# Kernel optimization log

Measured on AMD Instinct MI355X. Metric: run time of the kernel, lower is better.

Reference implementation:

```python
import jax, jax.numpy as jnp
import numpy as np

B, S, D, H = 4, 2048, 1024, 16
HD = D // H  # head dim = 64


def setup_inputs() -> dict:
    key = jax.random.key(0)
    k1, k2, k3 = jax.random.split(key, 3)
    scale = 1.0 / np.sqrt(D).astype(np.float32)
    x = jax.random.normal(k1, (B, S, D), dtype=jnp.float32)
    # q/k slices of nn.MultiheadAttention's in_proj (v and out_proj never
    # influence the returned values since x_t is discarded by forward)
    wq = jax.random.normal(k2, (D, D), dtype=jnp.float32) * scale
    wk = jax.random.normal(k3, (D, D), dtype=jnp.float32) * scale
    bq = jnp.zeros((D,), dtype=jnp.float32)
    bk = jnp.zeros((D,), dtype=jnp.float32)
    # 8 contiguous scale blocks of 256 tokens; last boundary == S
    scales_idx = (jnp.arange(1, 9, dtype=jnp.int64) * (S // 8))
    return {"x": x, "wq": wq, "wk": wk, "bq": bq, "bk": bk,
            "scales_idx": scales_idx}


def reference(x, wq, wk, bq, bk, scales_idx):
    b, s, d = x.shape
    # project q, k and split heads: [B, H, S, HD]
    q = (x @ wq.T + bq).reshape(b, s, H, HD).transpose(0, 2, 1, 3)
    k = (x @ wk.T + bk).reshape(b, s, H, HD).transpose(0, 2, 1, 3)
    inv_sqrt_hd = jnp.asarray(1.0 / np.sqrt(HD), dtype=x.dtype)
    scores = jnp.einsum('bhqd,bhkd->bhqk', q, k) * inv_sqrt_hd  # [B,H,S,S]
    # block-diagonal mask: token i belongs to the block whose right boundary
    # is the first scales_idx entry strictly greater than i
    pos = jnp.arange(s)
    seg = jnp.searchsorted(scales_idx, pos, side='right')  # [S]
    allowed = seg[:, None] == seg[None, :]                  # [S,S] bool
    scores = jnp.where(allowed[None, None], scores, -jnp.inf)
    w = jax.nn.softmax(scores, axis=-1)  # every row has >=1 allowed entry
    weights_attn = jnp.mean(w, axis=1)   # average over heads -> [B,S,S]
    return (x, weights_attn)
```

## Files before the change

kernel.cpp:

```cpp
#include <hip/hip_runtime.h>
#include <hip/hip_bf16.h>
#include <math.h>

#define BB 4
#define SS 2048
#define DD 1024
#define HH 16
#define HD 64
#define MM (BB*SS)
#define NN (2*DD)
#define BK 64
#define NKT 16

typedef __attribute__((ext_vector_type(8))) short short8;
typedef __attribute__((ext_vector_type(4))) float f32x4;
typedef unsigned short ushort_t;

__device__ __forceinline__ void gload16(const void* g, void* l) {
    __builtin_amdgcn_global_load_lds((const __attribute__((address_space(1))) unsigned int*)g,
                                     (__attribute__((address_space(3))) unsigned int*)l,
                                     16, 0, 0);
}

__global__ __launch_bounds__(256)
void copy_cast(const float* __restrict__ x, float* __restrict__ out_x,
               __hip_bfloat16* __restrict__ xb, int n8)
{
    int i = blockIdx.x * 256 + threadIdx.x;
    if (i >= n8) return;
    const float4* s = (const float4*)x + (size_t)i * 2;
    float4 a = s[0], b = s[1];
    float4* o = (float4*)out_x + (size_t)i * 2;
    o[0] = a; o[1] = b;
    __hip_bfloat16 tmp[8];
    tmp[0] = __float2bfloat16(a.x); tmp[1] = __float2bfloat16(a.y);
    tmp[2] = __float2bfloat16(a.z); tmp[3] = __float2bfloat16(a.w);
    tmp[4] = __float2bfloat16(b.x); tmp[5] = __float2bfloat16(b.y);
    tmp[6] = __float2bfloat16(b.z); tmp[7] = __float2bfloat16(b.w);
    *(float4*)&xb[(size_t)i * 8] = *(float4*)tmp;
}

__global__ __launch_bounds__(256)
void cast_w(const float* __restrict__ wq, const float* __restrict__ wk,
            __hip_bfloat16* __restrict__ wb)
{
    const int half = (DD * DD) / 8;
    int i = blockIdx.x * 256 + threadIdx.x;
    if (i >= 2 * half) return;
    const float* src = (i < half) ? wq : wk;
    int j = (i < half) ? i : i - half;
    const float4* s = (const float4*)src + (size_t)j * 2;
    float4 a = s[0], b = s[1];
    __hip_bfloat16 tmp[8];
    tmp[0] = __float2bfloat16(a.x); tmp[1] = __float2bfloat16(a.y);
    tmp[2] = __float2bfloat16(a.z); tmp[3] = __float2bfloat16(a.w);
    tmp[4] = __float2bfloat16(b.x); tmp[5] = __float2bfloat16(b.y);
    tmp[6] = __float2bfloat16(b.z); tmp[7] = __float2bfloat16(b.w);
    *(float4*)&wb[(size_t)i * 8] = *(float4*)tmp;
}

__device__ __forceinline__ void stage_A(const ushort_t* __restrict__ xb, ushort_t* Ab,
                                        int m0, int kt, int mh, int wv, int lane)
{
    #pragma unroll
    for (int it = 0; it < 2; ++it) {
        int rl0 = it * 64 + wv * 8;
        int r0 = (rl0 & 63) + ((rl0 >> 6) << 7) + mh * 64;
        int r  = r0 + (lane >> 3);
        int gch = (lane & 7) ^ (r & 7);
        gload16(xb + (size_t)(m0 + r) * DD + kt + gch * 8, Ab + r0 * 64);
    }
}

__device__ __forceinline__ void stage_Bt(const ushort_t* __restrict__ wb, ushort_t* Bb,
                                         int n0, int kt, int nh, int wv, int lane)
{
    #pragma unroll
    for (int it = 0; it < 2; ++it) {
        int rl0 = it * 64 + wv * 8;
        int r0 = (rl0 & 31) + ((rl0 >> 5) << 6) + nh * 32;
        int r  = r0 + (lane >> 3);
        int gch = (lane & 7) ^ (r & 7);
        gload16(wb + (size_t)(n0 + r) * DD + kt + gch * 8, Bb + r0 * 64);
    }
}

__global__ __launch_bounds__(512, 2)
void proj_mfma(const ushort_t* __restrict__ xb, const ushort_t* __restrict__ wb,
               const float* __restrict__ bq, const float* __restrict__ bk,
               __hip_bfloat16* __restrict__ Qb, __hip_bfloat16* __restrict__ Kb)
{
    __shared__ __align__(16) ushort_t As[2][256 * BK];
    __shared__ __align__(16) ushort_t Bs[2][256 * BK];

    const int t = threadIdx.x;
    const int wv = t >> 6, lane = t & 63, quad = lane >> 4, l15 = lane & 15;
    const int wr = wv >> 2, wc = wv & 3;
    const int m0 = blockIdx.x * 256, n0 = blockIdx.y * 256;

    f32x4 acc[8][4];
    #pragma unroll
    for (int mt = 0; mt < 8; ++mt)
        #pragma unroll
        for (int nt = 0; nt < 4; ++nt) acc[mt][nt] = (f32x4){0.f, 0.f, 0.f, 0.f};

    stage_Bt(wb, Bs[0], n0, 0, 0, wv, lane);
    stage_A (xb, As[0], m0, 0, 0, wv, lane);
    stage_A (xb, As[0], m0, 0, 1, wv, lane);
    stage_Bt(wb, Bs[0], n0, 0, 1, wv, lane);
    stage_Bt(wb, Bs[1], n0, BK, 0, wv, lane);
    stage_A (xb, As[1], m0, BK, 0, wv, lane);
    asm volatile("s_waitcnt vmcnt(4)" ::: "memory");
    __builtin_amdgcn_s_barrier();

    #pragma unroll 1
    for (int tt = 0; tt < NKT; ++tt) {
        ushort_t* Ac = As[tt & 1];
        ushort_t* Bc = Bs[tt & 1];
        ushort_t* An = As[(tt & 1) ^ 1];
        ushort_t* Bn = Bs[(tt & 1) ^ 1];
        short8 a[8][2], b[2][2];

        #pragma unroll
        for (int mt = 0; mt < 4; ++mt)
            #pragma unroll
            for (int ks = 0; ks < 2; ++ks) {
                int r = wr * 128 + mt * 16 + l15;
                int sl = r * 8 + ((ks * 4 + quad) ^ (r & 7));
                a[mt][ks] = *(const short8*)&Ac[sl * 8];
            }
        #pragma unroll
        for (int nt = 0; nt < 2; ++nt)
            #pragma unroll
            for (int ks = 0; ks < 2; ++ks) {
                int r = wc * 64 + nt * 16 + l15;
                int sl = r * 8 + ((ks * 4 + quad) ^ (r & 7));
                b[nt][ks] = *(const short8*)&Bc[sl * 8];
            }
        if (tt + 1 < NKT) stage_A(xb, An, m0, (tt + 1) * BK, 1, wv, lane);
        __builtin_amdgcn_s_barrier();
        asm volatile("s_waitcnt lgkmcnt(0)" ::: "memory");
        __builtin_amdgcn_sched_barrier(0);
        __builtin_amdgcn_s_setprio(1);
        #pragma unroll
        for (int mt = 0; mt < 4; ++mt)
            #pragma unroll
            for (int nt = 0; nt < 2; ++nt)
                #pragma unroll
                for (int ks = 0; ks < 2; ++ks)
                    acc[mt][nt] = __builtin_amdgcn_mfma_f32_16x16x32_bf16(
                        a[mt][ks], b[nt][ks], acc[mt][nt], 0, 0, 0);
        __builtin_amdgcn_s_setprio(0);
        __builtin_amdgcn_sched_barrier(0);
        __builtin_amdgcn_s_barrier();

        #pragma unroll
        for (int mt = 0; mt < 4; ++mt)
            #pragma unroll
            for (int ks = 0; ks < 2; ++ks) {
                int r = wr * 128 + 64 + mt * 16 + l15;
                int sl = r * 8 + ((ks * 4 + quad) ^ (r & 7));
                a[4 + mt][ks] = *(const short8*)&Ac[sl * 8];
            }
        if (tt + 1 < NKT) stage_Bt(wb, Bn, n0, (tt + 1) * BK, 1, wv, lane);
        __builtin_amdgcn_s_barrier();
        asm volatile("s_waitcnt lgkmcnt(0)" ::: "memory");
        __builtin_amdgcn_sched_barrier(0);
        __builtin_amdgcn_s_setprio(1);
        #pragma unroll
        for (int mt = 0; mt < 4; ++mt)
            #pragma unroll
            for (int nt = 0; nt < 2; ++nt)
                #pragma unroll
                for (int ks = 0; ks < 2; ++ks)
                    acc[4 + mt][nt] = __builtin_amdgcn_mfma_f32_16x16x32_bf16(
                        a[4 + mt][ks], b[nt][ks], acc[4 + mt][nt], 0, 0, 0);
        __builtin_amdgcn_s_setprio(0);
        __builtin_amdgcn_sched_barrier(0);
        __builtin_amdgcn_s_barrier();

        #pragma unroll
        for (int nt = 0; nt < 2; ++nt)
            #pragma unroll
            for (int ks = 0; ks < 2; ++ks) {
                int r = wc * 64 + 32 + nt * 16 + l15;
                int sl = r * 8 + ((ks * 4 + quad) ^ (r & 7));
                b[nt][ks] = *(const short8*)&Bc[sl * 8];
            }
        if (tt + 2 < NKT) stage_Bt(wb, Bc, n0, (tt + 2) * BK, 0, wv, lane);
        __builtin_amdgcn_s_barrier();
        asm volatile("s_waitcnt lgkmcnt(0)" ::: "memory");
        __builtin_amdgcn_sched_barrier(0);
        __builtin_amdgcn_s_setprio(1);
        #pragma unroll
        for (int mt = 0; mt < 4; ++mt)
            #pragma unroll
            for (int nt = 0; nt < 2; ++nt)
                #pragma unroll
                for (int ks = 0; ks < 2; ++ks)
                    acc[mt][2 + nt] = __builtin_amdgcn_mfma_f32_16x16x32_bf16(
                        a[mt][ks], b[nt][ks], acc[mt][2 + nt], 0, 0, 0);
        __builtin_amdgcn_s_setprio(0);
        __builtin_amdgcn_sched_barrier(0);
        __builtin_amdgcn_s_barrier();

        if (tt + 2 < NKT) stage_A(xb, Ac, m0, (tt + 2) * BK, 0, wv, lane);
        __builtin_amdgcn_s_barrier();
        asm volatile("s_waitcnt lgkmcnt(0)" ::: "memory");
        __builtin_amdgcn_sched_barrier(0);
        __builtin_amdgcn_s_setprio(1);
        #pragma unroll
        for (int mt = 0; mt < 4; ++mt)
            #pragma unroll
            for (int nt = 0; nt < 2; ++nt)
                #pragma unroll
                for (int ks = 0; ks < 2; ++ks)
                    acc[4 + mt][2 + nt] = __builtin_amdgcn_mfma_f32_16x16x32_bf16(
                        a[4 + mt][ks], b[nt][ks], acc[4 + mt][2 + nt], 0, 0, 0);
        __builtin_amdgcn_s_setprio(0);
        __builtin_amdgcn_sched_barrier(0);
        if (tt < NKT - 2)       asm volatile("s_waitcnt vmcnt(4)" ::: "memory");
        else if (tt == NKT - 2) asm volatile("s_waitcnt vmcnt(0)" ::: "memory");
        __builtin_amdgcn_s_barrier();
    }

    const bool isQ = (n0 < DD);
    const float* bias = isQ ? bq : bk;
    __hip_bfloat16* outp = isQ ? Qb : Kb;
    const int nc0 = (isQ ? n0 : n0 - DD) + wc * 64;
    #pragma unroll
    for (int nt = 0; nt < 4; ++nt) {
        const int nc = nc0 + nt * 16 + l15;
        const float bv = bias[nc];
        #pragma unroll
        for (int mt = 0; mt < 8; ++mt)
            #pragma unroll
            for (int reg = 0; reg < 4; ++reg) {
                int m = m0 + wr * 128 + mt * 16 + quad * 4 + reg;
                outp[(size_t)m * DD + nc] = __float2bfloat16(acc[mt][nt][reg] + bv);
            }
    }
}

__global__ __launch_bounds__(256, 1)
void attn_block(const ushort_t* __restrict__ Qb, const ushort_t* __restrict__ Kb,
                const int* __restrict__ scales, float* __restrict__ outw)
{
    __shared__ __align__(16) char smem[73728];
    ushort_t* KsB = (ushort_t*)smem;
    ushort_t* QsB = (ushort_t*)(smem + 65536);
    float (*comb)[256] = (float(*)[256])smem;

    const int bid = blockIdx.x;
    const int rt  = bid >> 5;
    const int blk = bid & 7, bb = (bid >> 3) & 3;
    const int start = blk ? scales[blk - 1] : 0;

    const int t = threadIdx.x;
    const int wv = t >> 6, lane = t & 63, quad = lane >> 4, l15 = lane & 15;
    const int rg = wv & 1, hg = wv >> 1;

    f32x4 accm[16];
    #pragma unroll
    for (int nt = 0; nt < 16; ++nt) accm[nt] = (f32x4){0.f, 0.f, 0.f, 0.f};

    const int qrow0 = start + rt * 32;

    for (int i = 0; i < 8; ++i) {
        __syncthreads();
        #pragma unroll
        for (int half = 0; half < 2; ++half) {
            const int h = half * 8 + i;
            ushort_t* Kl = KsB + half * (256 * 64);
            ushort_t* Ql = QsB + half * (32 * 64);
            #pragma unroll
            for (int round = 0; round < 8; ++round) {
                int c = round * 256 + t;
                int row = c >> 3, ch = c & 7;
                int gch = ch ^ (row & 7);
                gload16(Kb + (size_t)(bb * SS + start + row) * DD + h * HD + gch * 8,
                        Kl + ((size_t)round * 256 + wv * 64) * 8);
            }
            {
                int row = t >> 3, ch = t & 7;
                int gch = ch ^ (row & 7);
                gload16(Qb + (size_t)(bb * SS + qrow0 + row) * DD + h * HD + gch * 8,
                        Ql + ((size_t)wv * 64) * 8);
            }
        }
        __syncthreads();

        const ushort_t* Ks = KsB + hg * (256 * 64);
        const ushort_t* Qs = QsB + hg * (32 * 64);

        short8 af[2];
        #pragma unroll
        for (int ks = 0; ks < 2; ++ks) {
            int qr = rg * 16 + l15;
            int sl = qr * 8 + ((ks * 4 + quad) ^ (qr & 7));
            af[ks] = *(const short8*)&Qs[sl * 8];
        }
        f32x4 sc[16];
        #pragma unroll
        for (int nt = 0; nt < 16; ++nt) {
            sc[nt] = (f32x4){0.f, 0.f, 0.f, 0.f};
            #pragma unroll
            for (int ks = 0; ks < 2; ++ks) {
                int kr = nt * 16 + l15;
                int sl = kr * 8 + ((ks * 4 + quad) ^ (kr & 7));
                short8 bf = *(const short8*)&Ks[sl * 8];
                sc[nt] = __builtin_amdgcn_mfma_f32_16x16x32_bf16(af[ks], bf, sc[nt], 0, 0, 0);
            }
        }
        float rs[4] = {0.f, 0.f, 0.f, 0.f};
        #pragma unroll
        for (int nt = 0; nt < 16; ++nt) {
            #pragma unroll
            for (int r = 0; r < 4; ++r) {
                float p = __expf(sc[nt][r] * 0.125f);
                sc[nt][r] = p;
                rs[r] += p;
            }
        }
        #pragma unroll
        for (int r = 0; r < 4; ++r) {
            #pragma unroll
            for (int off = 1; off < 16; off <<= 1) rs[r] += __shfl_xor(rs[r], off, 64);
            rs[r] = 1.0f / rs[r];
        }
        #pragma unroll
        for (int nt = 0; nt < 16; ++nt)
            #pragma unroll
            for (int r = 0; r < 4; ++r) accm[nt][r] += sc[nt][r] * rs[r];
    }

    __syncthreads();
    if (hg == 0) {
        #pragma unroll
        for (int nt = 0; nt < 16; ++nt)
            #pragma unroll
            for (int r = 0; r < 4; ++r)
                comb[rg * 16 + quad * 4 + r][nt * 16 + l15] = accm[nt][r];
    }
    __syncthreads();
    if (hg == 1) {
        #pragma unroll
        for (int nt = 0; nt < 16; ++nt)
            #pragma unroll
            for (int r = 0; r < 4; ++r)
                comb[rg * 16 + quad * 4 + r][nt * 16 + l15] += accm[nt][r];
    }
    __syncthreads();

    const float s16 = 1.0f / (float)HH;
    const size_t orow0 = (size_t)bb * SS + qrow0;
    #pragma unroll
    for (int it = 0; it < 64; ++it) {
        int flat = it * 256 + t;
        int row = flat >> 9;
        int col = (flat & 511) * 4;
        float4 v = make_float4(0.f, 0.f, 0.f, 0.f);
        unsigned lc = (unsigned)(col - start);
        if (lc < 256u) {
            const float* c = &comb[row][lc];
            v = make_float4(c[0] * s16, c[1] * s16, c[2] * s16, c[3] * s16);
        }
        *(float4*)&outw[(orow0 + row) * SS + col] = v;
    }
}

extern "C" void kernel_launch(void* const* d_in, const int* in_sizes, int n_in,
                              void* d_out, int out_size, void* d_ws, size_t ws_size,
                              hipStream_t stream)
{
    const float* x  = (const float*)d_in[0];
    const float* wq = (const float*)d_in[1];
    const float* wk = (const float*)d_in[2];
    const float* bq = (const float*)d_in[3];
    const float* bk = (const float*)d_in[4];
    const int* scales = (const int*)d_in[5];

    float* out_x = (float*)d_out;
    float* out_w = out_x + (size_t)BB * SS * DD;

    char* w = (char*)d_ws;
    __hip_bfloat16* xb = (__hip_bfloat16*)(w);
    __hip_bfloat16* wb = (__hip_bfloat16*)(w + 16777216);
    __hip_bfloat16* Qb = (__hip_bfloat16*)(w + 20971520);
    __hip_bfloat16* Kb = (__hip_bfloat16*)(w + 37748736);

    copy_cast<<<4096, 256, 0, stream>>>(x, out_x, xb, (MM * DD) / 8);
    cast_w<<<1024, 256, 0, stream>>>(wq, wk, wb);

    dim3 pgrid(MM / 256, NN / 256);
    proj_mfma<<<pgrid, 512, 0, stream>>>((const ushort_t*)xb, (const ushort_t*)wb,
                                         bq, bk, Qb, Kb);

    attn_block<<<256, 256, 0, stream>>>((const ushort_t*)Qb, (const ushort_t*)Kb,
                                        scales, out_w);
}
```

Before: 208.0 us.

## Double-buffer K/Q staging in attention kernel and use nontemporal output stores

The attention kernel now double-buffers the per-head K and Q tiles in LDS, issuing the next head's async global-to-LDS loads before computing the current head, with a partial vmcnt wait and raw barriers in place of __syncthreads. This aims to hide global load latency behind MFMA and softmax work. Separately, the x copy and the large weights output use nontemporal stores to reduce cache pollution on streaming writes. LDS use doubles to 144 KB, which removes any chance of a second block per CU, and the hand-tuned vmcnt count depends on the exact number of loads issued per stage.

```diff
diff --git a/kernel.cpp b/kernel.cpp
--- a/kernel.cpp
+++ b/kernel.cpp
@@ -28,10 +28,11 @@
 {
     int i = blockIdx.x * 256 + threadIdx.x;
     if (i >= n8) return;
-    const float4* s = (const float4*)x + (size_t)i * 2;
-    float4 a = s[0], b = s[1];
-    float4* o = (float4*)out_x + (size_t)i * 2;
-    o[0] = a; o[1] = b;
+    const f32x4* s = (const f32x4*)x + (size_t)i * 2;
+    f32x4 a = s[0], b = s[1];
+    f32x4* o = (f32x4*)out_x + (size_t)i * 2;
+    __builtin_nontemporal_store(a, o);
+    __builtin_nontemporal_store(b, o + 1);
     __hip_bfloat16 tmp[8];
     tmp[0] = __float2bfloat16(a.x); tmp[1] = __float2bfloat16(a.y);
     tmp[2] = __float2bfloat16(a.z); tmp[3] = __float2bfloat16(a.w);
@@ -246,9 +247,7 @@
 void attn_block(const ushort_t* __restrict__ Qb, const ushort_t* __restrict__ Kb,
                 const int* __restrict__ scales, float* __restrict__ outw)
 {
-    __shared__ __align__(16) char smem[73728];
-    ushort_t* KsB = (ushort_t*)smem;
-    ushort_t* QsB = (ushort_t*)(smem + 65536);
+    __shared__ __align__(16) char smem[147456];
     float (*comb)[256] = (float(*)[256])smem;
 
     const int bid = blockIdx.x;
@@ -265,33 +264,44 @@
     for (int nt = 0; nt < 16; ++nt) accm[nt] = (f32x4){0.f, 0.f, 0.f, 0.f};
 
     const int qrow0 = start + rt * 32;
-
-    for (int i = 0; i < 8; ++i) {
-        __syncthreads();
+    const int brow  = bb * SS;
+
+    auto stageKQ = [&](int i, int buf) {
         #pragma unroll
         for (int half = 0; half < 2; ++half) {
             const int h = half * 8 + i;
-            ushort_t* Kl = KsB + half * (256 * 64);
-            ushort_t* Ql = QsB + half * (32 * 64);
+            ushort_t* Kl = (ushort_t*)(smem + (size_t)(buf * 2 + half) * 32768);
+            ushort_t* Ql = (ushort_t*)(smem + 131072 + (size_t)(buf * 2 + half) * 4096);
             #pragma unroll
             for (int round = 0; round < 8; ++round) {
                 int c = round * 256 + t;
                 int row = c >> 3, ch = c & 7;
                 int gch = ch ^ (row & 7);
-                gload16(Kb + (size_t)(bb * SS + start + row) * DD + h * HD + gch * 8,
+                gload16(Kb + (size_t)(brow + start + row) * DD + h * HD + gch * 8,
                         Kl + ((size_t)round * 256 + wv * 64) * 8);
             }
             {
                 int row = t >> 3, ch = t & 7;
                 int gch = ch ^ (row & 7);
-                gload16(Qb + (size_t)(bb * SS + qrow0 + row) * DD + h * HD + gch * 8,
+                gload16(Qb + (size_t)(brow + qrow0 + row) * DD + h * HD + gch * 8,
                         Ql + ((size_t)wv * 64) * 8);
             }
         }
-        __syncthreads();
-
-        const ushort_t* Ks = KsB + hg * (256 * 64);
-        const ushort_t* Qs = QsB + hg * (32 * 64);
+    };
+
+    stageKQ(0, 0);
+
+    for (int i = 0; i < 8; ++i) {
+        if (i < 7) {
+            stageKQ(i + 1, (i + 1) & 1);
+            asm volatile("s_waitcnt vmcnt(18)" ::: "memory");
+        } else {
+            asm volatile("s_waitcnt vmcnt(0)" ::: "memory");
+        }
+        __builtin_amdgcn_s_barrier();
+
+        const ushort_t* Ks = (const ushort_t*)(smem + (size_t)((i & 1) * 2 + hg) * 32768);
+        const ushort_t* Qs = (const ushort_t*)(smem + 131072 + (size_t)((i & 1) * 2 + hg) * 4096);
 
         short8 af[2];
         #pragma unroll
@@ -332,6 +342,8 @@
         for (int nt = 0; nt < 16; ++nt)
             #pragma unroll
             for (int r = 0; r < 4; ++r) accm[nt][r] += sc[nt][r] * rs[r];
+
+        __builtin_amdgcn_s_barrier();
     }
 
     __syncthreads();
@@ -359,13 +371,13 @@
         int flat = it * 256 + t;
         int row = flat >> 9;
         int col = (flat & 511) * 4;
-        float4 v = make_float4(0.f, 0.f, 0.f, 0.f);
+        f32x4 v = (f32x4){0.f, 0.f, 0.f, 0.f};
         unsigned lc = (unsigned)(col - start);
         if (lc < 256u) {
             const float* c = &comb[row][lc];
-            v = make_float4(c[0] * s16, c[1] * s16, c[2] * s16, c[3] * s16);
-        }
-        *(float4*)&outw[(orow0 + row) * SS + col] = v;
+            v = (f32x4){c[0] * s16, c[1] * s16, c[2] * s16, c[3] * s16};
+        }
+        __builtin_nontemporal_store(v, (f32x4*)&outw[(orow0 + row) * SS + col]);
     }
 }
 
```

Measured after the change: 208.0 us. About the same (+0.0%).
